# Kernel tuning notes

Hardware: AMD Instinct MI355X
Metric: run time of the kernel (lower is better)

## Reference

```python
import jax, jax.numpy as jnp
import numpy as np

N, E, F_IN, D, R, L = 50000, 800000, 128, 64, 8, 3


def setup_inputs() -> dict:
    key = jax.random.key(0)
    ks = jax.random.split(key, 8)
    x = jax.random.normal(ks[0], (N, F_IN), dtype=jnp.float32)
    edge_index = jax.random.randint(ks[1], (2, E), 0, N)
    dist = jax.random.uniform(ks[2], (E,), dtype=jnp.float32)
    etype = jax.random.randint(ks[3], (E,), 0, R).astype(jnp.float32)
    edge_attr = jnp.stack([dist, etype], axis=1)  # [E, 2]: col0 distance, col1 relation id
    W_in = jax.random.normal(ks[4], (F_IN, D), dtype=jnp.float32) / np.float32(np.sqrt(F_IN))
    b_in = jnp.zeros((D,), jnp.float32)
    W_rel = jax.random.normal(ks[5], (L, R, D, D), dtype=jnp.float32) / np.float32(np.sqrt(D))
    W_root = jax.random.normal(ks[6], (L, D, D), dtype=jnp.float32) / np.float32(np.sqrt(D))
    b_conv = jnp.zeros((L, D), jnp.float32)
    return dict(x=x, edge_index=edge_index, edge_attr=edge_attr, W_in=W_in,
                b_in=b_in, W_rel=W_rel, W_root=W_root, b_conv=b_conv)


def rgcn_conv(h, src, dst, etype, Wr, Wroot, b):
    # PyG RGCNConv: per-relation MEAN aggregation + root weight + bias.
    # Composite segment id (dst, relation) -> one scatter over N*R segments.
    seg = dst * R + etype  # [E]
    msg = h[src]  # [E, D] gather
    s = jax.ops.segment_sum(msg, seg, num_segments=N * R)            # [N*R, D]
    cnt = jax.ops.segment_sum(jnp.ones((E,), h.dtype), seg, num_segments=N * R)
    mean = (s / jnp.maximum(cnt, 1.0)[:, None]).reshape(N, R, D)     # [N, R, D]
    return jnp.einsum('nrd,rde->ne', mean, Wr) + h @ Wroot + b


def reference(x, edge_index, edge_attr, W_in, b_in, W_rel, W_root, b_conv):
    edge_type = edge_attr[:, 1].astype(jnp.int32)
    edge_distance = edge_attr[:, 0]
    src, dst = edge_index[0], edge_index[1]
    h = jax.nn.relu(x @ W_in + b_in)
    for l in range(L):
        h = jax.nn.relu(rgcn_conv(h, src, dst, edge_type, W_rel[l], W_root[l], b_conv[l]))
    return h, edge_distance
```

## Files before the change

kernel.cpp:

```cpp
#include <hip/hip_runtime.h>

#define NN 50000
#define EE 800000
#define FIN 128
#define DD 64
#define RR 8
#define LL 3

#define ND (NN*DD)
#define NR (NN*RR)

#define SB 1024
#define NSB ((NR + SB - 1) / SB)
#define ECAP 1024
#define ASF 68
#define KB 576

typedef __attribute__((ext_vector_type(8))) short bf16x8;
typedef __attribute__((ext_vector_type(4))) float f32x4;

__device__ __forceinline__ unsigned short f2bf(float x) {
  unsigned u = __float_as_uint(x);
  u += 0x7fff + ((u >> 16) & 1);
  return (unsigned short)(u >> 16);
}
__device__ __forceinline__ void split_bf(float x, short& h, short& l) {
  unsigned short hu = f2bf(x);
  float hf = __uint_as_float((unsigned)hu << 16);
  h = (short)hu;
  l = (short)f2bf(x - hf);
}

__global__ void k_prep(const float* __restrict__ W_rel,
                       const float* __restrict__ W_root,
                       const float* __restrict__ W_in,
                       short* __restrict__ Btp, short* __restrict__ Wt) {
  const int idx = blockIdx.x * 256 + threadIdx.x;
  if (idx < LL * DD * KB) {
    const int k = idx % KB, n = (idx / KB) % DD, l = idx / (KB * DD);
    float w;
    if (k < 512) w = W_rel[(((size_t)l*RR + (k >> 6))*DD + (k & 63))*DD + n];
    else         w = W_root[((size_t)l*DD + (k - 512))*DD + n];
    short hi, lo; split_bf(w, hi, lo);
    Btp[((size_t)(l*2+0)*DD + n)*KB + k] = hi;
    Btp[((size_t)(l*2+1)*DD + n)*KB + k] = lo;
  }
  if (idx < DD * FIN) {
    const int k = idx % FIN, n = idx / FIN;
    float w = W_in[(size_t)k*DD + n];
    short hi, lo; split_bf(w, hi, lo);
    Wt[((size_t)0*DD + n)*FIN + k] = hi;
    Wt[((size_t)1*DD + n)*FIN + k] = lo;
  }
}

__global__ __launch_bounds__(256) void k_input_mfma(
    const float* __restrict__ x, const short* __restrict__ Wt,
    const float* __restrict__ b, float* __restrict__ h) {
  __shared__ short Ah[DD * 136];
  __shared__ short Al[DD * 136];
  const int t = threadIdx.x;
  const int lane = t & 63, wv = t >> 6;
  const int lr = lane & 15, lc = lane >> 4;
  const int n0 = blockIdx.x * 64;

  {
    const int row = t >> 2, cb = (t & 3) * 32;
    const int n = n0 + row;
    #pragma unroll
    for (int i = 0; i < 8; ++i) {
      const int col = cb + i * 4;
      float4 v = make_float4(0.f,0.f,0.f,0.f);
      if (n < NN) v = *(const float4*)(x + (size_t)n*FIN + col);
      short h0,l0,h1,l1,h2,l2,h3,l3;
      split_bf(v.x,h0,l0); split_bf(v.y,h1,l1);
      split_bf(v.z,h2,l2); split_bf(v.w,h3,l3);
      unsigned long long ph = (unsigned short)h0 | ((unsigned long long)(unsigned short)h1<<16)
          | ((unsigned long long)(unsigned short)h2<<32) | ((unsigned long long)(unsigned short)h3<<48);
      unsigned long long pl = (unsigned short)l0 | ((unsigned long long)(unsigned short)l1<<16)
          | ((unsigned long long)(unsigned short)l2<<32) | ((unsigned long long)(unsigned short)l3<<48);
      *(unsigned long long*)&Ah[row*136 + col] = ph;
      *(unsigned long long*)&Al[row*136 + col] = pl;
    }
  }
  __syncthreads();

  const int m0 = wv * 16;
  f32x4 acc[4];
  #pragma unroll
  for (int nt = 0; nt < 4; ++nt) acc[nt] = (f32x4){0.f,0.f,0.f,0.f};
  const int aoff = (m0 + lr)*136 + lc*8;
  int boff[4];
  #pragma unroll
  for (int nt = 0; nt < 4; ++nt) boff[nt] = (nt*16 + lr)*FIN + lc*8;

  #pragma unroll
  for (int ks = 0; ks < 4; ++ks) {
    const bf16x8 ah = *(const bf16x8*)&Ah[aoff + ks*32];
    const bf16x8 al = *(const bf16x8*)&Al[aoff + ks*32];
    #pragma unroll
    for (int nt = 0; nt < 4; ++nt) {
      const bf16x8 bh = *(const bf16x8*)(Wt + boff[nt] + ks*32);
      const bf16x8 bl = *(const bf16x8*)(Wt + DD*FIN + boff[nt] + ks*32);
      acc[nt] = __builtin_amdgcn_mfma_f32_16x16x32_bf16(ah, bh, acc[nt], 0, 0, 0);
      acc[nt] = __builtin_amdgcn_mfma_f32_16x16x32_bf16(al, bh, acc[nt], 0, 0, 0);
      acc[nt] = __builtin_amdgcn_mfma_f32_16x16x32_bf16(ah, bl, acc[nt], 0, 0, 0);
    }
  }
  #pragma unroll
  for (int nt = 0; nt < 4; ++nt) {
    const float bb = b[nt*16 + lr];
    #pragma unroll
    for (int i = 0; i < 4; ++i) {
      const int m = n0 + m0 + lc*4 + i;
      if (m < NN) h[(size_t)m*DD + nt*16 + lr] = fmaxf(acc[nt][i] + bb, 0.f);
    }
  }
}

__global__ void k_hist(const int* __restrict__ ei, const float* __restrict__ ea,
                       int* __restrict__ rp, float* __restrict__ outd) {
  const int e = blockIdx.x * 256 + threadIdx.x;
  if (e >= EE) return;
  const float2 v = *(const float2*)(ea + 2*e);
  outd[e] = v.x;
  atomicAdd(&rp[(int)v.y * NN + ei[EE + e]], 1);
}

__global__ __launch_bounds__(256) void k_scan1(int* __restrict__ rp,
                                               int* __restrict__ part) {
  __shared__ int ls[256];
  const int t = threadIdx.x;
  const int base = blockIdx.x * SB + t * 4;
  int v[4] = {0,0,0,0};
  #pragma unroll
  for (int i = 0; i < 4; ++i)
    if (base + i < NR) v[i] = rp[base + i];
  const int tsum = v[0] + v[1] + v[2] + v[3];
  ls[t] = tsum; __syncthreads();
  #pragma unroll
  for (int off = 1; off < 256; off <<= 1) {
    int x = (t >= off) ? ls[t - off] : 0;
    __syncthreads();
    ls[t] += x;
    __syncthreads();
  }
  if (t == 255) part[blockIdx.x] = ls[255];
  int run = ls[t] - tsum;
  #pragma unroll
  for (int i = 0; i < 4; ++i) {
    if (base + i < NR) rp[base + i] = run;
    run += v[i];
  }
}

__global__ __launch_bounds__(512) void k_scan2(int* __restrict__ part) {
  __shared__ int ls[512];
  const int t = threadIdx.x;
  const int v = (t < NSB) ? part[t] : 0;
  ls[t] = v; __syncthreads();
  #pragma unroll
  for (int off = 1; off < 512; off <<= 1) {
    int x = (t >= off) ? ls[t - off] : 0;
    __syncthreads();
    ls[t] += x;
    __syncthreads();
  }
  if (t < NSB) part[t] = ls[t] - v;
}

__global__ __launch_bounds__(256) void k_scan3(int* __restrict__ rp,
                                               const int* __restrict__ part,
                                               int* __restrict__ fill) {
  const int base = blockIdx.x * SB + threadIdx.x * 4;
  const int off = part[blockIdx.x];
  #pragma unroll
  for (int i = 0; i < 4; ++i)
    if (base + i < NR) {
      const int r = rp[base + i] + off;
      rp[base + i] = r;
      fill[base + i] = r;
    }
  if (blockIdx.x == 0 && threadIdx.x == 0) rp[NR] = EE;
}

__global__ void k_reorder(const int* __restrict__ ei, const float* __restrict__ ea,
                          int* __restrict__ fill, unsigned short* __restrict__ eidx) {
  const int e = blockIdx.x * 256 + threadIdx.x;
  if (e >= EE) return;
  const int key = (int)ea[2*e + 1] * NN + ei[EE + e];
  const int pos = atomicAdd(&fill[key], 1);
  eidx[pos] = (unsigned short)ei[e];
}

__global__ __launch_bounds__(256, 4) void k_layer(
    const float* __restrict__ h, const unsigned short* __restrict__ eidx,
    const int* __restrict__ rp, const short* __restrict__ Btp,
    const float* __restrict__ bias, float* __restrict__ outh) {
  __shared__ float Af[4][16 * ASF];
  __shared__ unsigned short els[ECAP];
  __shared__ int rpls[RR][33];
  __shared__ int baseL[RR + 1];

  const int t = threadIdx.x;
  const int lane = t & 63, wv = t >> 6;
  const int pair = wv >> 1, half = wv & 1;
  const int lr = lane & 15, lc = lane >> 4;
  const int n0 = blockIdx.x * 32;
  const int j0 = pair * 16;
  const float* hl = h + lane;

  for (int i = t; i < RR * 33; i += 256) {
    const int kk = i / 33, j = i - kk * 33;
    int g = n0 + j; if (g > NN) g = NN;
    rpls[kk][j] = rp[kk * NN + g];
  }
  __syncthreads();
  if (t == 0) {
    int s = 0;
    #pragma unroll
    for (int k = 0; k < RR; ++k) { baseL[k] = s; s += rpls[k][32] - rpls[k][0]; }
    baseL[RR] = s;
  }
  __syncthreads();
  const bool fit = baseL[RR] <= ECAP;
  if (fit) {
    for (int k = 0; k < RR; ++k) {
      const int g0 = rpls[k][0], sp = rpls[k][32] - g0, b0 = baseL[k];
      for (int i = t; i < sp; i += 256) els[b0 + i] = eidx[g0 + i];
    }
  }
  __syncthreads();

  float* Aw = Af[wv];

  auto gather = [&](int kk) {
    const int ebeg = rpls[kk][j0], eend = rpls[kk][j0 + 16];
    int j = j0;
    int nxt = rpls[kk][j0 + 1];
    float acc = 0.f;
    auto flush = [&]() {
      const int cnt = nxt - rpls[kk][j];
      float m = (cnt > 1) ? acc * (1.0f / (float)cnt) : acc;
      Aw[(j - j0) * ASF + lane] = m;
    };
    auto proc = [&](float v, int e2) {
      while (e2 >= nxt) { flush(); acc = 0.f; ++j; nxt = rpls[kk][j + 1]; }
      acc += v;
    };
    auto scan = [&](auto srcAt) {
      int e = ebeg;
      for (; e + 15 < eend; e += 16) {
        int s[16]; float v[16];
        #pragma unroll
        for (int i = 0; i < 16; ++i) s[i] = srcAt(e + i);
        #pragma unroll
        for (int i = 0; i < 16; ++i) v[i] = hl[(size_t)s[i] * DD];
        #pragma unroll
        for (int i = 0; i < 16; ++i) proc(v[i], e + i);
      }
      if (e + 7 < eend) {
        int s[8]; float v[8];
        #pragma unroll
        for (int i = 0; i < 8; ++i) s[i] = srcAt(e + i);
        #pragma unroll
        for (int i = 0; i < 8; ++i) v[i] = hl[(size_t)s[i] * DD];
        #pragma unroll
        for (int i = 0; i < 8; ++i) proc(v[i], e + i);
        e += 8;
      }
      for (; e < eend; ++e) proc(hl[(size_t)srcAt(e) * DD], e);
    };
    if (fit) {
      const int lb2 = baseL[kk] - rpls[kk][0];
      scan([&](int e) { return (int)els[lb2 + e]; });
    } else {
      scan([&](int e) { return (int)eidx[e]; });
    }
    while (true) {
      flush();
      acc = 0.f; ++j;
      if (j >= j0 + 16) break;
      nxt = rpls[kk][j + 1];
    }
  };
  auto root_stage = [&]() {
    for (int jj = 0; jj < 16; jj += 4) {
      float v[4];
      #pragma unroll
      for (int i = 0; i < 4; ++i) {
        const int n = n0 + j0 + jj + i;
        v[i] = (n < NN) ? h[(size_t)n * DD + lane] : 0.f;
      }
      #pragma unroll
      for (int i = 0; i < 4; ++i) Aw[(jj + i) * ASF + lane] = v[i];
    }
  };

  f32x4 acc4[4];
  #pragma unroll
  for (int nt = 0; nt < 4; ++nt) acc4[nt] = (f32x4){0.f,0.f,0.f,0.f};
  int boff[4];
  #pragma unroll
  for (int nt = 0; nt < 4; ++nt) boff[nt] = (nt*16 + lr)*KB + lc*8;
  const short* Blo = Btp + (size_t)DD * KB;
  const float* arow = Aw + lr * ASF + lc * 8;

  auto mfma_slice = [&](int koff) {
    #pragma unroll
    for (int ks = 0; ks < 2; ++ks) {
      const f32x4 a0 = *(const f32x4*)(arow + ks*32);
      const f32x4 a1 = *(const f32x4*)(arow + ks*32 + 4);
      bf16x8 ah, al;
      #pragma unroll
      for (int i = 0; i < 4; ++i) {
        short hb, lb;
        split_bf(a0[i], hb, lb); ah[i] = hb;     al[i] = lb;
        split_bf(a1[i], hb, lb); ah[4 + i] = hb; al[4 + i] = lb;
      }
      #pragma unroll
      for (int nt = 0; nt < 4; ++nt) {
        const bf16x8 bh = *(const bf16x8*)(Btp + boff[nt] + koff + ks*32);
        const bf16x8 bl = *(const bf16x8*)(Blo + boff[nt] + koff + ks*32);
        acc4[nt] = __builtin_amdgcn_mfma_f32_16x16x32_bf16(ah, bh, acc4[nt], 0, 0, 0);
        acc4[nt] = __builtin_amdgcn_mfma_f32_16x16x32_bf16(al, bh, acc4[nt], 0, 0, 0);
        acc4[nt] = __builtin_amdgcn_mfma_f32_16x16x32_bf16(ah, bl, acc4[nt], 0, 0, 0);
      }
    }
  };

  #pragma unroll 1
  for (int kx = 0; kx < 4; ++kx) {
    const int kk = half * 4 + kx;
    gather(kk);
    mfma_slice(kk * 64);
  }
  if (!half) {
    root_stage();
    mfma_slice(512);
  } else {
    #pragma unroll
    for (int nt = 0; nt < 4; ++nt)
      #pragma unroll
      for (int i = 0; i < 4; ++i)
        Aw[(lc*4 + i) * ASF + nt*16 + lr] = acc4[nt][i];
  }
  __syncthreads();
  if (!half) {
    const float* Pw = Af[wv + 1];
    #pragma unroll
    for (int nt = 0; nt < 4; ++nt) {
      const float bb = bias[nt*16 + lr];
      #pragma unroll
      for (int i = 0; i < 4; ++i) {
        const int m = n0 + j0 + lc*4 + i;
        if (m < NN)
          outh[(size_t)m*DD + nt*16 + lr] =
              fmaxf(acc4[nt][i] + Pw[(lc*4 + i) * ASF + nt*16 + lr] + bb, 0.f);
      }
    }
  }
}

extern "C" void kernel_launch(void* const* d_in, const int* in_sizes, int n_in,
                              void* d_out, int out_size, void* d_ws, size_t ws_size,
                              hipStream_t stream) {
  const float* x      = (const float*)d_in[0];
  const int*   ei     = (const int*)d_in[1];
  const float* ea     = (const float*)d_in[2];
  const float* W_in   = (const float*)d_in[3];
  const float* b_in   = (const float*)d_in[4];
  const float* W_rel  = (const float*)d_in[5];
  const float* W_root = (const float*)d_in[6];
  const float* b_conv = (const float*)d_in[7];
  float* out = (float*)d_out;

  char* ws = (char*)d_ws;
  float*          hA   = (float*)(ws);
  float*          hB   = (float*)(ws + 12800000);
  int*            rp   = (int*)  (ws + 25600000);
  int*            fill = (int*)  (ws + 27200256);
  unsigned short* eidx = (unsigned short*)(ws + 28800256);
  int*            part = (int*)  (ws + 30400256);
  short*          Btp  = (short*)(ws + 30402304);
  short*          Wt   = (short*)(ws + 30844672);

  k_prep<<<(LL*DD*KB + 255)/256, 256, 0, stream>>>(W_rel, W_root, W_in, Btp, Wt);
  k_input_mfma<<<(NN + 63)/64, 256, 0, stream>>>(x, Wt, b_in, hA);

  hipMemsetAsync(rp, 0, (size_t)NR*4, stream);
  k_hist<<<(EE + 255)/256, 256, 0, stream>>>(ei, ea, rp, out + (size_t)ND);
  k_scan1<<<NSB, 256, 0, stream>>>(rp, part);
  k_scan2<<<1, 512, 0, stream>>>(part);
  k_scan3<<<NSB, 256, 0, stream>>>(rp, part, fill);
  k_reorder<<<(EE + 255)/256, 256, 0, stream>>>(ei, ea, fill, eidx);

  const int NBL = (NN + 31) / 32;
  const float* hin = hA;
  for (int l = 0; l < LL; ++l) {
    float* hout = (l == 2) ? out : ((l == 0) ? hB : hA);
    k_layer<<<NBL, 256, 0, stream>>>(hin, eidx, rp,
        Btp + (size_t)l*2*DD*KB, b_conv + (size_t)l*DD, hout);
    hin = hout;
  }
}
```

Before: 388.9 us.

## Merge preprocessing kernels to cut launch count and fold scan2 into scan3

Merges weight prep into the histogram kernel and runs the first scan pass inside the input-projection kernel as extra blocks, so independent work shares launches. The single-block scan2 is removed: each scan3 block now sums the preceding partials itself with a shared-memory reduction. This cuts the preprocessing launches from seven to four and removes one serial single-block step. In exchange every scan block redundantly reads up to ~400 partials, and the layer loop is written out by hand.

```diff
diff --git a/kernel.cpp b/kernel.cpp
--- a/kernel.cpp
+++ b/kernel.cpp
@@ -15,6 +15,9 @@
 #define ECAP 1024
 #define ASF 68
 #define KB 576
+#define HB ((EE + 255) / 256)
+#define PB ((LL*DD*KB + 255) / 256)
+#define IB ((NN + 63) / 64)
 
 typedef __attribute__((ext_vector_type(8))) short bf16x8;
 typedef __attribute__((ext_vector_type(4))) float f32x4;
@@ -31,35 +34,75 @@
   l = (short)f2bf(x - hf);
 }
 
-__global__ void k_prep(const float* __restrict__ W_rel,
-                       const float* __restrict__ W_root,
-                       const float* __restrict__ W_in,
-                       short* __restrict__ Btp, short* __restrict__ Wt) {
-  const int idx = blockIdx.x * 256 + threadIdx.x;
-  if (idx < LL * DD * KB) {
-    const int k = idx % KB, n = (idx / KB) % DD, l = idx / (KB * DD);
-    float w;
-    if (k < 512) w = W_rel[(((size_t)l*RR + (k >> 6))*DD + (k & 63))*DD + n];
-    else         w = W_root[((size_t)l*DD + (k - 512))*DD + n];
-    short hi, lo; split_bf(w, hi, lo);
-    Btp[((size_t)(l*2+0)*DD + n)*KB + k] = hi;
-    Btp[((size_t)(l*2+1)*DD + n)*KB + k] = lo;
-  }
-  if (idx < DD * FIN) {
-    const int k = idx % FIN, n = idx / FIN;
-    float w = W_in[(size_t)k*DD + n];
-    short hi, lo; split_bf(w, hi, lo);
-    Wt[((size_t)0*DD + n)*FIN + k] = hi;
-    Wt[((size_t)1*DD + n)*FIN + k] = lo;
-  }
-}
-
-__global__ __launch_bounds__(256) void k_input_mfma(
+__global__ void k_hist_prep(const int* __restrict__ ei, const float* __restrict__ ea,
+                            int* __restrict__ rp, float* __restrict__ outd,
+                            const float* __restrict__ W_rel,
+                            const float* __restrict__ W_root,
+                            const float* __restrict__ W_in,
+                            short* __restrict__ Btp, short* __restrict__ Wt) {
+  const int b = blockIdx.x;
+  if (b < HB) {
+    const int e = b * 256 + threadIdx.x;
+    if (e >= EE) return;
+    const float2 v = *(const float2*)(ea + 2*e);
+    outd[e] = v.x;
+    atomicAdd(&rp[(int)v.y * NN + ei[EE + e]], 1);
+  } else {
+    const int idx = (b - HB) * 256 + threadIdx.x;
+    if (idx < LL * DD * KB) {
+      const int k = idx % KB, n = (idx / KB) % DD, l = idx / (KB * DD);
+      float w;
+      if (k < 512) w = W_rel[(((size_t)l*RR + (k >> 6))*DD + (k & 63))*DD + n];
+      else         w = W_root[((size_t)l*DD + (k - 512))*DD + n];
+      short hi, lo; split_bf(w, hi, lo);
+      Btp[((size_t)(l*2+0)*DD + n)*KB + k] = hi;
+      Btp[((size_t)(l*2+1)*DD + n)*KB + k] = lo;
+    }
+    if (idx < DD * FIN) {
+      const int k = idx % FIN, n = idx / FIN;
+      float w = W_in[(size_t)k*DD + n];
+      short hi, lo; split_bf(w, hi, lo);
+      Wt[((size_t)0*DD + n)*FIN + k] = hi;
+      Wt[((size_t)1*DD + n)*FIN + k] = lo;
+    }
+  }
+}
+
+__global__ __launch_bounds__(256) void k_input_scan1(
     const float* __restrict__ x, const short* __restrict__ Wt,
-    const float* __restrict__ b, float* __restrict__ h) {
+    const float* __restrict__ b, float* __restrict__ h,
+    int* __restrict__ rp, int* __restrict__ part) {
   __shared__ short Ah[DD * 136];
   __shared__ short Al[DD * 136];
   const int t = threadIdx.x;
+
+  if (blockIdx.x >= IB) {
+    int* ls = (int*)Ah;
+    const int bb = blockIdx.x - IB;
+    const int base = bb * SB + t * 4;
+    int v[4] = {0,0,0,0};
+    #pragma unroll
+    for (int i = 0; i < 4; ++i)
+      if (base + i < NR) v[i] = rp[base + i];
+    const int tsum = v[0] + v[1] + v[2] + v[3];
+    ls[t] = tsum; __syncthreads();
+    #pragma unroll
+    for (int off = 1; off < 256; off <<= 1) {
+      int xv = (t >= off) ? ls[t - off] : 0;
+      __syncthreads();
+      ls[t] += xv;
+      __syncthreads();
+    }
+    if (t == 255) part[bb] = ls[255];
+    int run = ls[t] - tsum;
+    #pragma unroll
+    for (int i = 0; i < 4; ++i) {
+      if (base + i < NR) rp[base + i] = run;
+      run += v[i];
+    }
+    return;
+  }
+
   const int lane = t & 63, wv = t >> 6;
   const int lr = lane & 15, lc = lane >> 4;
   const int n0 = blockIdx.x * 64;
@@ -118,70 +161,30 @@
   }
 }
 
-__global__ void k_hist(const int* __restrict__ ei, const float* __restrict__ ea,
-                       int* __restrict__ rp, float* __restrict__ outd) {
-  const int e = blockIdx.x * 256 + threadIdx.x;
-  if (e >= EE) return;
-  const float2 v = *(const float2*)(ea + 2*e);
-  outd[e] = v.x;
-  atomicAdd(&rp[(int)v.y * NN + ei[EE + e]], 1);
-}
-
-__global__ __launch_bounds__(256) void k_scan1(int* __restrict__ rp,
-                                               int* __restrict__ part) {
+__global__ __launch_bounds__(256) void k_scan23(int* __restrict__ rp,
+                                                const int* __restrict__ part,
+                                                int* __restrict__ fill) {
   __shared__ int ls[256];
   const int t = threadIdx.x;
-  const int base = blockIdx.x * SB + t * 4;
-  int v[4] = {0,0,0,0};
-  #pragma unroll
-  for (int i = 0; i < 4; ++i)
-    if (base + i < NR) v[i] = rp[base + i];
-  const int tsum = v[0] + v[1] + v[2] + v[3];
-  ls[t] = tsum; __syncthreads();
-  #pragma unroll
-  for (int off = 1; off < 256; off <<= 1) {
-    int x = (t >= off) ? ls[t - off] : 0;
+  const int bb = blockIdx.x;
+  int s = 0;
+  for (int i = t; i < bb; i += 256) s += part[i];
+  ls[t] = s; __syncthreads();
+  #pragma unroll
+  for (int off = 128; off > 0; off >>= 1) {
+    if (t < off) ls[t] += ls[t + off];
     __syncthreads();
-    ls[t] += x;
-    __syncthreads();
-  }
-  if (t == 255) part[blockIdx.x] = ls[255];
-  int run = ls[t] - tsum;
-  #pragma unroll
-  for (int i = 0; i < 4; ++i) {
-    if (base + i < NR) rp[base + i] = run;
-    run += v[i];
-  }
-}
-
-__global__ __launch_bounds__(512) void k_scan2(int* __restrict__ part) {
-  __shared__ int ls[512];
-  const int t = threadIdx.x;
-  const int v = (t < NSB) ? part[t] : 0;
-  ls[t] = v; __syncthreads();
-  #pragma unroll
-  for (int off = 1; off < 512; off <<= 1) {
-    int x = (t >= off) ? ls[t - off] : 0;
-    __syncthreads();
-    ls[t] += x;
-    __syncthreads();
-  }
-  if (t < NSB) part[t] = ls[t] - v;
-}
-
-__global__ __launch_bounds__(256) void k_scan3(int* __restrict__ rp,
-                                               const int* __restrict__ part,
-                                               int* __restrict__ fill) {
-  const int base = blockIdx.x * SB + threadIdx.x * 4;
-  const int off = part[blockIdx.x];
+  }
+  const int off0 = ls[0];
+  const int base = bb * SB + t * 4;
   #pragma unroll
   for (int i = 0; i < 4; ++i)
     if (base + i < NR) {
-      const int r = rp[base + i] + off;
+      const int r = rp[base + i] + off0;
       rp[base + i] = r;
       fill[base + i] = r;
     }
-  if (blockIdx.x == 0 && threadIdx.x == 0) rp[NR] = EE;
+  if (bb == 0 && t == 0) rp[NR] = EE;
 }
 
 __global__ void k_reorder(const int* __restrict__ ei, const float* __restrict__ ea,
@@ -385,22 +388,18 @@
   short*          Btp  = (short*)(ws + 30402304);
   short*          Wt   = (short*)(ws + 30844672);
 
-  k_prep<<<(LL*DD*KB + 255)/256, 256, 0, stream>>>(W_rel, W_root, W_in, Btp, Wt);
-  k_input_mfma<<<(NN + 63)/64, 256, 0, stream>>>(x, Wt, b_in, hA);
-
   hipMemsetAsync(rp, 0, (size_t)NR*4, stream);
-  k_hist<<<(EE + 255)/256, 256, 0, stream>>>(ei, ea, rp, out + (size_t)ND);
-  k_scan1<<<NSB, 256, 0, stream>>>(rp, part);
-  k_scan2<<<1, 512, 0, stream>>>(part);
-  k_scan3<<<NSB, 256, 0, stream>>>(rp, part, fill);
-  k_reorder<<<(EE + 255)/256, 256, 0, stream>>>(ei, ea, fill, eidx);
+  k_hist_prep<<<HB + PB, 256, 0, stream>>>(ei, ea, rp, out + (size_t)ND,
+                                           W_rel, W_root, W_in, Btp, Wt);
+  k_input_scan1<<<IB + NSB, 256, 0, stream>>>(x, Wt, b_in, hA, rp, part);
+  k_scan23<<<NSB, 256, 0, stream>>>(rp, part, fill);
+  k_reorder<<<HB, 256, 0, stream>>>(ei, ea, fill, eidx);
 
   const int NBL = (NN + 31) / 32;
-  const float* hin = hA;
-  for (int l = 0; l < LL; ++l) {
-    float* hout = (l == 2) ? out : ((l == 0) ? hB : hA);
-    k_layer<<<NBL, 256, 0, stream>>>(hin, eidx, rp,
-        Btp + (size_t)l*2*DD*KB, b_conv + (size_t)l*DD, hout);
-    hin = hout;
-  }
-}
+  k_layer<<<NBL, 256, 0, stream>>>(hA, eidx, rp,
+      Btp + (size_t)0*2*DD*KB, b_conv + (size_t)0*DD, hB);
+  k_layer<<<NBL, 256, 0, stream>>>(hB, eidx, rp,
+      Btp + (size_t)1*2*DD*KB, b_conv + (size_t)1*DD, hA);
+  k_layer<<<NBL, 256, 0, stream>>>(hA, eidx, rp,
+      Btp + (size_t)2*2*DD*KB, b_conv + (size_t)2*DD, out);
+}
```

New measurement: 378.1 us, median of 2. 2.8% less time.
